# Kernel optimization log

Hardware: AMD Instinct MI355X
Metric: run time of the kernel (lower is better)

## Reference

```python
import math
import jax, jax.numpy as jnp
import numpy as np

SM_K = 5

def make_sm_kernel(kernel_size=SM_K, sigma_e=1.2, sigma_i=1.4):
    center = kernel_size // 2
    xx, yy = jnp.meshgrid(jnp.arange(kernel_size, dtype=jnp.float32),
                          jnp.arange(kernel_size, dtype=jnp.float32), indexing='ij')
    xx = xx - center
    yy = yy - center
    g_e = jnp.exp(-(xx ** 2 + yy ** 2) / (2.0 * sigma_e ** 2))
    g_i = jnp.exp(-(xx ** 2 + yy ** 2) / (2.0 * sigma_i ** 2))
    dog = g_e / (2.0 * math.pi * sigma_e ** 2) - g_i / (2.0 * math.pi * sigma_i ** 2)
    return dog / dog[center, center]  # (5,5), normalized so center == 1


def setup_inputs() -> dict:
    key = jax.random.key(0)
    k1, k2 = jax.random.split(key)
    B, Cin, H, W = 16, 64, 128, 128
    Cout, K = 64, 5
    x = jax.random.normal(k1, (B, Cin, H, W), dtype=jnp.float32)
    weight_range = 25.0 / math.sqrt(Cin * K * K)
    weight = weight_range * jnp.abs(jax.random.normal(k2, (Cout, Cin, K, K), dtype=jnp.float32))
    return {"x": x, "weight": weight}


def reference(x, weight):
    PAD = 2
    dn = ('NCHW', 'OIHW', 'NCHW')
    Cout = weight.shape[0]
    K = weight.shape[-1]

    # symmetric_pad -> F.pad reflect
    xp = jnp.pad(x, ((0, 0), (0, 0), (PAD, PAD), (PAD, PAD)), mode='reflect')

    # w = weight.abs(); F.normalize(w, p=2, dim=1): L2 norm over in_channels per (o, kh, kw)
    w = jnp.abs(weight)
    nrm = jnp.sqrt(jnp.sum(w * w, axis=1, keepdims=True))
    w_n = w / jnp.maximum(nrm, 1e-12)

    # cosine similarity: conv with normalized weights / input patch norm
    conv = jax.lax.conv_general_dilated(xp, w_n, (1, 1), 'VALID', dimension_numbers=dn)
    # conv(x^2, ones_like(w)) yields identical values for every output channel;
    # compute once with a single-output-channel ones kernel and broadcast.
    ones_k = jnp.ones((1, x.shape[1], K, K), dtype=x.dtype)
    xsq_sum = jax.lax.conv_general_dilated(xp * xp, ones_k, (1, 1), 'VALID', dimension_numbers=dn)
    y = conv / jnp.sqrt(xsq_sum + 1e-8)  # (B, Cout, H, W)

    # surround modulation: depthwise conv with fixed 5x5 DoG kernel, padding 2
    sm = make_sm_kernel()
    sm_k = jnp.broadcast_to(sm[None, None].astype(y.dtype), (Cout, 1, SM_K, SM_K))
    y = jax.lax.conv_general_dilated(y, sm_k, (1, 1), [(SM_K // 2, SM_K // 2)] * 2,
                                     dimension_numbers=dn, feature_group_count=Cout)
    return y
```

## Files before the change

### kernel.cpp

```cpp
#include <hip/hip_runtime.h>
#include <hip/hip_bf16.h>
#include <math.h>

#define B_   16
#define CIN  64
#define COUT 64
#define H_   128
#define W_   128
#define KK   25
#define HW   (H_ * W_)
#define XT_PLANE ((size_t)B_ * HW * 32)
#define WTS ((size_t)COUT * H_ * 32)

typedef short  bf16x8 __attribute__((ext_vector_type(8)));
typedef short  s16x4  __attribute__((ext_vector_type(4)));
typedef float  f32x16 __attribute__((ext_vector_type(16)));
typedef float  f32x4  __attribute__((ext_vector_type(4)));
typedef float  f32x2  __attribute__((ext_vector_type(2)));

__device__ __forceinline__ short f2bs(float v) {
    __hip_bfloat16 h = __float2bfloat16(v);
    return *reinterpret_cast<short*>(&h);
}
__device__ __forceinline__ float bs2f(short s) {
    unsigned int u = ((unsigned int)(unsigned short)s) << 16;
    return __uint_as_float(u);
}

__global__ __launch_bounds__(256) void k_prep(const float* __restrict__ x,
                                              const float* __restrict__ w,
                                              short* __restrict__ xt,
                                              float* __restrict__ xsqg,
                                              short* __restrict__ wnb2) {
    const int tid = threadIdx.x;

    if (blockIdx.z == B_) {
        if (blockIdx.x != 0 || blockIdx.y >= COUT) return;
        __shared__ float wl[CIN * KK];
        __shared__ float inv[KK];
        const int o = blockIdx.y;

        for (int idx = tid; idx < CIN * KK; idx += 256)
            wl[idx] = w[(size_t)o * (CIN * KK) + idx];
        __syncthreads();
        if (tid < KK) {
            float s = 0.f;
            #pragma unroll 8
            for (int i = 0; i < CIN; ++i) { float v = wl[i * KK + tid]; s += v * v; }
            inv[tid] = 1.f / fmaxf(sqrtf(s), 1e-12f);
        }
        __syncthreads();
        const int tt = o >> 5, n = o & 31;
        for (int idx = tid; idx < CIN * KK; idx += 256) {
            int ci = idx & 63, kk = idx >> 6;
            int ks = ci >> 4, q = (ci >> 3) & 1, j = ci & 7;
            int l = q * 32 + n;
            wnb2[((size_t)((kk * 4 + ks) * 2 + tt) * 64 + l) * 8 + j] =
                f2bs(fabsf(wl[ci * KK + kk]) * inv[kk]);
        }
        return;
    }

    __shared__ float tile[64][65];
    __shared__ float ps[8][64];
    const int b = blockIdx.z, h = blockIdx.y, w0 = blockIdx.x * 64;

    const float* xb = x + (size_t)b * CIN * HW + h * W_ + w0;
    {
        int c4 = tid & 15, g = tid >> 4;
        #pragma unroll
        for (int k = 0; k < 4; ++k) {
            int ci = g * 4 + k;
            *(f32x4*)&tile[ci][c4 * 4] =
                *(const f32x4*)&xb[(size_t)ci * HW + c4 * 4];
        }
    }
    __syncthreads();

    const size_t pixbase = (size_t)b * HW + h * W_ + w0;
    {
        int c8 = tid & 7;
        int half = c8 >> 2, sl = c8 & 3;
        short* dp = xt + (size_t)half * XT_PLANE;
        #pragma unroll
        for (int rep = 0; rep < 2; ++rep) {
            int p = (tid >> 3) + rep * 32;
            bf16x8 v; float sq = 0.f;
            #pragma unroll
            for (int j = 0; j < 8; ++j) {
                float f = tile[c8 * 8 + j][p];
                sq += f * f;
                v[j] = f2bs(f);
            }
            ps[c8][p] = sq;
            *(bf16x8*)&dp[(pixbase + p) * 32 + sl * 8] = v;
        }
    }
    __syncthreads();
    if (tid < 64) {
        float a = 0.f;
        #pragma unroll
        for (int c8 = 0; c8 < 8; ++c8) a += ps[c8][tid];
        xsqg[pixbase + tid] = a;
    }
}

#define XP 40
#define NR 12
#define NC 36
#define NS (NR * NC)
#define TP 264

__global__ __launch_bounds__(256, 4) void k_conv(const short* __restrict__ xt,
                                                 const float* __restrict__ xsqg,
                                                 const short* __restrict__ wnb2,
                                                 short* __restrict__ t2) {
    __shared__ short xin[NS * XP];
    __shared__ float s2win[NS];
    __shared__ int   soff[NS];
    __shared__ float xsq[256];

    const int tid  = threadIdx.x;
    const int lane = tid & 63;
    const int wv   = tid >> 6;
    const int n    = lane & 31;
    const int q    = lane >> 5;
    const int b    = blockIdx.z;
    const int h0   = blockIdx.y * 8;
    const int wt   = blockIdx.x;
    const int w0   = wt * 32;

    const size_t pixbase = (size_t)b * HW;

    for (int s = tid; s < NS; s += 256) {
        int r = s / NC, c = s - r * NC;
        int hh = h0 - 2 + r; hh = hh < 0 ? -hh : (hh > H_ - 1 ? 2 * (H_ - 1) - hh : hh);
        int ww = w0 - 2 + c; ww = ww < 0 ? -ww : (ww > W_ - 1 ? 2 * (W_ - 1) - ww : ww);
        int off = hh * W_ + ww;
        soff[s] = off;
        s2win[s] = xsqg[pixbase + off];
    }
    __syncthreads();

    {
        int hr = tid >> 5, cl = tid & 31;
        float a = 0.f;
        #pragma unroll
        for (int kh = 0; kh < 5; ++kh)
            #pragma unroll
            for (int kw = 0; kw < 5; ++kw)
                a += s2win[(hr + kh) * NC + cl + kw];
        xsq[tid] = a;
    }

    const short* wb = wnb2 + (size_t)lane * 8;

    f32x16 acc00, acc01, acc10, acc11;
    #pragma unroll
    for (int i = 0; i < 16; ++i) { acc00[i] = 0.f; acc01[i] = 0.f; acc10[i] = 0.f; acc11[i] = 0.f; }

    #pragma unroll
    for (int half = 0; half < 2; ++half) {
        const short* xph = xt + (size_t)half * XT_PLANE + pixbase * 32;
        for (int i = tid; i < NS * 4; i += 256) {
            int s = i >> 2, c8 = i & 3;
            *(bf16x8*)&xin[s * XP + c8 * 8] =
                *(const bf16x8*)&xph[(size_t)soff[s] * 32 + c8 * 8];
        }
        __syncthreads();

        #pragma unroll 5
        for (int kk = 0; kk < KK; ++kk) {
            const int kh = kk / 5, kw = kk % 5;
            const int sp0 = (2 * wv + kh) * NC + n + kw;
            #pragma unroll
            for (int ks2 = 0; ks2 < 2; ++ks2) {
                const int ks = half * 2 + ks2;
                const int ko = ks2 * 16 + q * 8;
                bf16x8 a0 = *(const bf16x8*)&xin[sp0 * XP + ko];
                bf16x8 a1 = *(const bf16x8*)&xin[(sp0 + NC) * XP + ko];
                bf16x8 b0 = *(const bf16x8*)&wb[(size_t)((kk * 4 + ks) * 2 + 0) * 512];
                bf16x8 b1 = *(const bf16x8*)&wb[(size_t)((kk * 4 + ks) * 2 + 1) * 512];
                acc00 = __builtin_amdgcn_mfma_f32_32x32x16_bf16(a0, b0, acc00, 0, 0, 0);
                acc01 = __builtin_amdgcn_mfma_f32_32x32x16_bf16(a0, b1, acc01, 0, 0, 0);
                acc10 = __builtin_amdgcn_mfma_f32_32x32x16_bf16(a1, b0, acc10, 0, 0, 0);
                acc11 = __builtin_amdgcn_mfma_f32_32x32x16_bf16(a1, b1, acc11, 0, 0, 0);
            }
        }
        __syncthreads();
    }

    short* trans = xin;
    const int hrA = 2 * wv, hrB = 2 * wv + 1;
    #pragma unroll
    for (int g4 = 0; g4 < 4; ++g4) {
        int wc0 = 8 * g4 + 4 * q;
        s16x4 v00, v01, v10, v11;
        #pragma unroll
        for (int j = 0; j < 4; ++j) {
            float ia = rsqrtf(xsq[hrA * 32 + wc0 + j] + 1e-8f);
            float ib = rsqrtf(xsq[hrB * 32 + wc0 + j] + 1e-8f);
            v00[j] = f2bs(acc00[4 * g4 + j] * ia);
            v01[j] = f2bs(acc01[4 * g4 + j] * ia);
            v10[j] = f2bs(acc10[4 * g4 + j] * ib);
            v11[j] = f2bs(acc11[4 * g4 + j] * ib);
        }
        *(s16x4*)&trans[n * TP        + hrA * 32 + wc0] = v00;
        *(s16x4*)&trans[(32 + n) * TP + hrA * 32 + wc0] = v01;
        *(s16x4*)&trans[n * TP        + hrB * 32 + wc0] = v10;
        *(s16x4*)&trans[(32 + n) * TP + hrB * 32 + wc0] = v11;
    }
    __syncthreads();

    short* tbase = t2 + ((size_t)(b * 4 + wt) * COUT) * (H_ * 32);
    #pragma unroll
    for (int u = tid; u < 512; u += 256) {
        int oc = u >> 3, hr = u & 7;
        const short* src = &trans[oc * TP + hr * 32];
        short* dst = tbase + ((size_t)oc * H_ + h0 + hr) * 32;
        float4 a0 = *(const float4*)(src);
        float4 a1 = *(const float4*)(src + 8);
        float4 a2 = *(const float4*)(src + 16);
        float4 a3 = *(const float4*)(src + 24);
        *(float4*)(dst)      = a0;
        *(float4*)(dst + 8)  = a1;
        *(float4*)(dst + 16) = a2;
        *(float4*)(dst + 24) = a3;
    }
}

__global__ __launch_bounds__(256) void k_dog(const short* __restrict__ t2,
                                             float* __restrict__ out) {
    __shared__ float tile[68 * 132];
    __shared__ float sm_s[25];
    const int bo  = blockIdx.y;
    const int h0  = blockIdx.x * 64;
    const int tid = threadIdx.x;

    if (tid < 25) {
        const float se2 = 2.f * 1.2f * 1.2f;
        const float si2 = 2.f * 1.4f * 1.4f;
        const float twopi = 6.28318530717958647692f;
        const float ae = 1.f / (twopi * 1.2f * 1.2f);
        const float ai = 1.f / (twopi * 1.4f * 1.4f);
        const float c0 = ae - ai;
        int dx = tid / 5 - 2, dy = tid % 5 - 2;
        float r2 = (float)(dx * dx + dy * dy);
        sm_s[tid] = (ae * expf(-r2 / se2) - ai * expf(-r2 / si2)) / c0;
    }

    const int bb = bo >> 6, oc = bo & 63;
    const short* base = t2 + ((size_t)(bb * 4) * COUT + oc) * (H_ * 32);
    for (int idx = tid; idx < 68 * 16; idx += 256) {
        int rr = idx >> 4, g = idx & 15;
        int hh = h0 - 2 + rr;
        float v[8];
        if (hh >= 0 && hh < H_) {
            int wtile = g >> 2, c = g & 3;
            bf16x8 a = *(const bf16x8*)&base[(size_t)wtile * WTS + (size_t)hh * 32 + c * 8];
            #pragma unroll
            for (int j = 0; j < 8; ++j) v[j] = bs2f(a[j]);
        } else {
            #pragma unroll
            for (int j = 0; j < 8; ++j) v[j] = 0.f;
        }
        float* dst = &tile[rr * 132 + 2 + g * 8];
        *(f32x2*)(dst)     = (f32x2){v[0], v[1]};
        *(f32x4*)(dst + 2) = (f32x4){v[2], v[3], v[4], v[5]};
        *(f32x2*)(dst + 6) = (f32x2){v[6], v[7]};
    }
    for (int idx = tid; idx < 68 * 4; idx += 256) {
        int rr = idx >> 2, c = idx & 3;
        tile[rr * 132 + (c < 2 ? c : 128 + c)] = 0.f;
    }
    __syncthreads();

    float smr[25];
    #pragma unroll
    for (int kk = 0; kk < 25; ++kk) smr[kk] = sm_s[kk];

    const int cq = tid & 31;
    const int r0 = tid >> 5;
    #pragma unroll
    for (int rr = 0; rr < 8; ++rr) {
        int r = r0 + 8 * rr;
        float s0 = 0.f, s1 = 0.f, s2 = 0.f, s3 = 0.f;
        #pragma unroll
        for (int kh = 0; kh < 5; ++kh) {
            const float* row = &tile[(r + kh) * 132 + cq * 4];
            f32x4 v0 = *(const f32x4*)(row);
            f32x4 v1 = *(const f32x4*)(row + 4);
            float vv[8] = { v0[0], v0[1], v0[2], v0[3], v1[0], v1[1], v1[2], v1[3] };
            #pragma unroll
            for (int kw = 0; kw < 5; ++kw) {
                float cf = smr[kh * 5 + kw];
                s0 += cf * vv[kw];
                s1 += cf * vv[kw + 1];
                s2 += cf * vv[kw + 2];
                s3 += cf * vv[kw + 3];
            }
        }
        float4 o4 = make_float4(s0, s1, s2, s3);
        *(float4*)&out[((size_t)bo * H_ + h0 + r) * W_ + cq * 4] = o4;
    }
}

extern "C" void kernel_launch(void* const* d_in, const int* in_sizes, int n_in,
                              void* d_out, int out_size, void* d_ws, size_t ws_size,
                              hipStream_t stream) {
    const float* x = (const float*)d_in[0];
    const float* w = (const float*)d_in[1];

    short* t2 = (short*)d_ws;

    short* xt    = (short*)d_out;
    float* xsqg  = (float*)((char*)d_out + 33554432);
    short* wnb2  = (short*)((char*)d_out + (size_t)67108864 - 204800);

    dim3 gx(W_ / 64, H_, B_ + 1);
    k_prep<<<gx, 256, 0, stream>>>(x, w, xt, xsqg, wnb2);

    dim3 g2(W_ / 32, H_ / 8, B_);
    k_conv<<<g2, 256, 0, stream>>>(xt, xsqg, wnb2, t2);

    dim3 g3(H_ / 64, B_ * COUT);
    k_dog<<<g3, 256, 0, stream>>>(t2, (float*)d_out);
}
```

Before: 189.9 us.

## Double-buffer input staging with direct global-to-LDS loads in conv kernel

Replaces the two-half synchronous register-staged input loading with four 16-channel quarters staged through a double-buffered LDS pool. Loads use global_load_lds so data goes straight to shared memory, and the next quarter is prefetched while MFMAs consume the current one. The padded stride of 40 shorts is dropped for a dense 16-short layout, which may bring LDS bank conflicts, and there are now four barriers instead of two.

```diff
diff --git a/kernel.cpp b/kernel.cpp
--- a/kernel.cpp
+++ b/kernel.cpp
@@ -26,6 +26,11 @@
     unsigned int u = ((unsigned int)(unsigned short)s) << 16;
     return __uint_as_float(u);
 }
+__device__ __forceinline__ void gload_lds16(const short* g, short* l) {
+    __builtin_amdgcn_global_load_lds(
+        (const __attribute__((address_space(1))) void*)g,
+        (__attribute__((address_space(3))) void*)l, 16, 0, 0);
+}
 
 __global__ __launch_bounds__(256) void k_prep(const float* __restrict__ x,
                                               const float* __restrict__ w,
@@ -105,20 +110,22 @@
     }
 }
 
-#define XP 40
 #define NR 12
 #define NC 36
 #define NS (NR * NC)
+#define NCH (NS * 2)
+#define QBUF 8192
 #define TP 264
 
 __global__ __launch_bounds__(256, 4) void k_conv(const short* __restrict__ xt,
                                                  const float* __restrict__ xsqg,
                                                  const short* __restrict__ wnb2,
                                                  short* __restrict__ t2) {
-    __shared__ short xin[NS * XP];
-    __shared__ float s2win[NS];
-    __shared__ int   soff[NS];
-    __shared__ float xsq[256];
+    __shared__ __align__(16) short pool[18624];
+    short* xin   = pool;
+    float* s2win = (float*)&pool[16384];
+    int*   soff  = (int*)&pool[17248];
+    float* xsq   = (float*)&pool[18112];
 
     const int tid  = threadIdx.x;
     const int lane = tid & 63;
@@ -153,44 +160,51 @@
         xsq[tid] = a;
     }
 
+    auto stage = [&](int qtr, int bs) {
+        const short* xph = xt + (size_t)(qtr >> 1) * XT_PLANE + pixbase * 32
+                              + (qtr & 1) * 16;
+        #pragma unroll
+        for (int k = 0; k < 4; ++k) {
+            int i = k * 256 + tid;
+            int ic = i < NCH ? i : NCH - 1;
+            int s = ic >> 1, c = ic & 1;
+            const short* src = xph + (size_t)soff[s] * 32 + c * 8;
+            short* dst = xin + bs * QBUF + (k * 256 + wv * 64) * 8;
+            gload_lds16(src, dst);
+        }
+    };
+
     const short* wb = wnb2 + (size_t)lane * 8;
 
     f32x16 acc00, acc01, acc10, acc11;
     #pragma unroll
     for (int i = 0; i < 16; ++i) { acc00[i] = 0.f; acc01[i] = 0.f; acc10[i] = 0.f; acc11[i] = 0.f; }
 
-    #pragma unroll
-    for (int half = 0; half < 2; ++half) {
-        const short* xph = xt + (size_t)half * XT_PLANE + pixbase * 32;
-        for (int i = tid; i < NS * 4; i += 256) {
-            int s = i >> 2, c8 = i & 3;
-            *(bf16x8*)&xin[s * XP + c8 * 8] =
-                *(const bf16x8*)&xph[(size_t)soff[s] * 32 + c8 * 8];
-        }
-        __syncthreads();
+    stage(0, 0);
+    __syncthreads();
+
+    for (int qtr = 0; qtr < 4; ++qtr) {
+        const int bs = qtr & 1;
+        if (qtr < 3) stage(qtr + 1, bs ^ 1);
 
         #pragma unroll 5
         for (int kk = 0; kk < KK; ++kk) {
             const int kh = kk / 5, kw = kk % 5;
             const int sp0 = (2 * wv + kh) * NC + n + kw;
-            #pragma unroll
-            for (int ks2 = 0; ks2 < 2; ++ks2) {
-                const int ks = half * 2 + ks2;
-                const int ko = ks2 * 16 + q * 8;
-                bf16x8 a0 = *(const bf16x8*)&xin[sp0 * XP + ko];
-                bf16x8 a1 = *(const bf16x8*)&xin[(sp0 + NC) * XP + ko];
-                bf16x8 b0 = *(const bf16x8*)&wb[(size_t)((kk * 4 + ks) * 2 + 0) * 512];
-                bf16x8 b1 = *(const bf16x8*)&wb[(size_t)((kk * 4 + ks) * 2 + 1) * 512];
-                acc00 = __builtin_amdgcn_mfma_f32_32x32x16_bf16(a0, b0, acc00, 0, 0, 0);
-                acc01 = __builtin_amdgcn_mfma_f32_32x32x16_bf16(a0, b1, acc01, 0, 0, 0);
-                acc10 = __builtin_amdgcn_mfma_f32_32x32x16_bf16(a1, b0, acc10, 0, 0, 0);
-                acc11 = __builtin_amdgcn_mfma_f32_32x32x16_bf16(a1, b1, acc11, 0, 0, 0);
-            }
+            const int ka = bs * QBUF + q * 8;
+            bf16x8 a0 = *(const bf16x8*)&xin[ka + sp0 * 16];
+            bf16x8 a1 = *(const bf16x8*)&xin[ka + (sp0 + NC) * 16];
+            bf16x8 b0 = *(const bf16x8*)&wb[(size_t)((kk * 4 + qtr) * 2 + 0) * 512];
+            bf16x8 b1 = *(const bf16x8*)&wb[(size_t)((kk * 4 + qtr) * 2 + 1) * 512];
+            acc00 = __builtin_amdgcn_mfma_f32_32x32x16_bf16(a0, b0, acc00, 0, 0, 0);
+            acc01 = __builtin_amdgcn_mfma_f32_32x32x16_bf16(a0, b1, acc01, 0, 0, 0);
+            acc10 = __builtin_amdgcn_mfma_f32_32x32x16_bf16(a1, b0, acc10, 0, 0, 0);
+            acc11 = __builtin_amdgcn_mfma_f32_32x32x16_bf16(a1, b1, acc11, 0, 0, 0);
         }
         __syncthreads();
     }
 
-    short* trans = xin;
+    short* trans = pool;
     const int hrA = 2 * wv, hrB = 2 * wv + 1;
     #pragma unroll
     for (int g4 = 0; g4 < 4; ++g4) {
```

Measured after the change: 190.7 us. No clear change (+0.4%).
